# Kernel optimization log

Hardware: AMD Instinct MI355X
Metric: run time of the kernel (lower is better)

## Reference

```python
import jax, jax.numpy as jnp
import numpy as np

OBS, ACT, LAT, H = 64, 32, 25, 5
B = 8192
SUP_H = 64


def setup_inputs() -> dict:
    key = jax.random.key(0)
    ks = jax.random.split(key, 12)
    s = 0.1
    inp = {
        'obs': jax.random.normal(ks[0], (B, OBS), jnp.float32),
        # supervisor FeedForward: OBS -> 64 -> 64 -> LAT, ReLU hidden, Sigmoid output
        'sw1': jax.random.normal(ks[1], (OBS, SUP_H), jnp.float32) * s,
        'sb1': jnp.zeros((SUP_H,), jnp.float32),
        'sw2': jax.random.normal(ks[2], (SUP_H, SUP_H), jnp.float32) * s,
        'sb2': jnp.zeros((SUP_H,), jnp.float32),
        'sw3': jax.random.normal(ks[3], (SUP_H, LAT), jnp.float32) * s,
        'sb3': jnp.zeros((LAT,), jnp.float32),
        # OBS*ACT tiny reflex FeedForwards 1 -> H -> 1, stacked into batched params
        'rw1': jax.random.normal(ks[4], (OBS, ACT, H), jnp.float32) * s,
        'rb1': jnp.zeros((OBS, ACT, H), jnp.float32),
        'rw2': jax.random.normal(ks[5], (OBS, ACT, H), jnp.float32) * s,
        'rb2': jnp.zeros((OBS, ACT), jnp.float32),
        # activation matrix (LAT, OBS, ACT)
        'act_matrix': jnp.ones((LAT, OBS, ACT), jnp.float32),
    }
    return inp


def reference(obs, sw1, sb1, sw2, sb2, sw3, sb3, rw1, rb1, rw2, rb2, act_matrix):
    # supervisor: (B, LAT) sigmoid latent activations
    h = jax.nn.relu(obs @ sw1 + sb1)
    h = jax.nn.relu(h @ sw2 + sb2)
    latent = jax.nn.sigmoid(h @ sw3 + sb3)

    # reflex gating: (B, LAT) x (LAT, OBS, ACT) -> (B, OBS, ACT), softmax over ACT
    logits = jnp.einsum('bl,loa->boa', latent, act_matrix)
    reflex_acts = jax.nn.softmax(logits, axis=-1)

    # all OBS*ACT tiny 1->H->1 MLPs, batched: input is obs[:, o] (scalar per net)
    # hidden: (B, OBS, ACT, H)
    rh = jax.nn.relu(obs[:, :, None, None] * rw1[None] + rb1[None])
    reflex_out = jnp.einsum('boah,oah->boa', rh, rw2) + rb2[None]  # (B, OBS, ACT)

    # weighted sum over obs dim -> (B, ACT)
    return jnp.sum(reflex_out * reflex_acts, axis=1)
```

## Files before the change

kernel.cpp:

```cpp
#include <hip/hip_runtime.h>


#define TOBS 64
#define TACT 32
#define TLAT 25
#define TH   5
#define TB   8192
#define BT   16
#define NCH  16
#define ATS  28
#define WTS  20
#define HSTR 68

#define DPP_ADD(x, ctrl) \
  ((x) + __builtin_bit_cast(float, __builtin_amdgcn_update_dpp( \
      0, __builtin_bit_cast(int, (x)), (ctrl), 0xF, 0xF, true)))

__device__ __forceinline__ float halfwave_sum(float x) {
    x = DPP_ADD(x, 0xB1);
    x = DPP_ADD(x, 0x4E);
    x = DPP_ADD(x, 0x141);
    x = DPP_ADD(x, 0x140);
    int y = __builtin_amdgcn_ds_swizzle(__builtin_bit_cast(int, x), 0x401F);
    return x + __builtin_bit_cast(float, y);
}

__device__ __forceinline__ float sigmoidf_(float x) {
    return 1.0f / (1.0f + __expf(-x));
}

__global__ __launch_bounds__(256, 2)
void reflex_fused(const float* __restrict__ obs,
                  const float* __restrict__ sw1, const float* __restrict__ sb1,
                  const float* __restrict__ sw2, const float* __restrict__ sb2,
                  const float* __restrict__ sw3, const float* __restrict__ sb3,
                  const float* __restrict__ rw1, const float* __restrict__ rb1,
                  const float* __restrict__ rw2, const float* __restrict__ rb2,
                  const float* __restrict__ am,  float* __restrict__ out)
{
    __shared__ __align__(16) float obs_s[BT * HSTR];
    __shared__ __align__(16) float lat_s[BT * 26];
    __shared__ __align__(16) union {
        struct { float h1[BT * HSTR]; float h2[BT * HSTR]; } p1;
        struct { float At[2][128 * ATS]; float W[2][128 * WTS]; } p2;
    } U;

    const int tid  = threadIdx.x;
    const int row0 = blockIdx.x * BT;

    {
        const int r = tid >> 4, f = tid & 15;
        *(float4*)&obs_s[r * HSTR + f * 4] =
            *(const float4*)&obs[(row0 + r) * TOBS + f * 4];
    }
    __syncthreads();

    {
        const int r = tid >> 4, j0 = (tid & 15) * 4;
        float4 acc = *(const float4*)&sb1[j0];
        #pragma unroll 8
        for (int k = 0; k < 64; ++k) {
            float x = obs_s[r * HSTR + k];
            const float4 w = *(const float4*)&sw1[k * 64 + j0];
            acc.x = fmaf(x, w.x, acc.x); acc.y = fmaf(x, w.y, acc.y);
            acc.z = fmaf(x, w.z, acc.z); acc.w = fmaf(x, w.w, acc.w);
        }
        *(float4*)&U.p1.h1[r * HSTR + j0] =
            make_float4(fmaxf(acc.x, 0.f), fmaxf(acc.y, 0.f),
                        fmaxf(acc.z, 0.f), fmaxf(acc.w, 0.f));
    }
    __syncthreads();

    {
        const int r = tid >> 4, j0 = (tid & 15) * 4;
        float4 acc = *(const float4*)&sb2[j0];
        #pragma unroll 8
        for (int k = 0; k < 64; ++k) {
            float x = U.p1.h1[r * HSTR + k];
            const float4 w = *(const float4*)&sw2[k * 64 + j0];
            acc.x = fmaf(x, w.x, acc.x); acc.y = fmaf(x, w.y, acc.y);
            acc.z = fmaf(x, w.z, acc.z); acc.w = fmaf(x, w.w, acc.w);
        }
        *(float4*)&U.p1.h2[r * HSTR + j0] =
            make_float4(fmaxf(acc.x, 0.f), fmaxf(acc.y, 0.f),
                        fmaxf(acc.z, 0.f), fmaxf(acc.w, 0.f));
    }
    __syncthreads();

    {
        const int r = tid >> 4, q = tid & 15;
        if (q < 13) {
            const int j = q * 2;
            float a0 = sb3[j];
            float a1 = (j + 1 < TLAT) ? sb3[j + 1] : 0.f;
            #pragma unroll 8
            for (int k = 0; k < 64; ++k) {
                float x = U.p1.h2[r * HSTR + k];
                a0 = fmaf(x, sw3[k * TLAT + j], a0);
                if (j + 1 < TLAT) a1 = fmaf(x, sw3[k * TLAT + j + 1], a1);
            }
            lat_s[r * 26 + j] = sigmoidf_(a0);
            if (j + 1 < TLAT) lat_s[r * 26 + j + 1] = sigmoidf_(a1);
        }
    }
    __syncthreads();

    const int a  = tid & 31;
    const int hw = tid >> 5;
    const int r0 = hw * 2, r1 = r0 + 1;

    float latA[TLAT], latB[TLAT];
    #pragma unroll
    for (int l = 0; l < TLAT; ++l) {
        latA[l] = lat_s[r0 * 26 + l];
        latB[l] = lat_s[r1 * 26 + l];
    }

    auto stage = [&](int c, int b) {
        if (tid < 128) {
            const int slot = tid >> 5, a_ = tid & 31;
            const int o = c * 4 + slot;
            const float* g = am + o * TACT + a_;
            float v0  = g[0*2048],  v1  = g[1*2048],  v2  = g[2*2048],  v3  = g[3*2048];
            float v4  = g[4*2048],  v5  = g[5*2048],  v6  = g[6*2048],  v7  = g[7*2048];
            float v8  = g[8*2048],  v9  = g[9*2048],  v10 = g[10*2048], v11 = g[11*2048];
            float v12 = g[12*2048], v13 = g[13*2048], v14 = g[14*2048], v15 = g[15*2048];
            float v16 = g[16*2048], v17 = g[17*2048], v18 = g[18*2048], v19 = g[19*2048];
            float v20 = g[20*2048], v21 = g[21*2048], v22 = g[22*2048], v23 = g[23*2048];
            float v24 = g[24*2048];
            float* d = &U.p2.At[b][tid * ATS];
            ((float4*)d)[0] = make_float4(v0,  v1,  v2,  v3);
            ((float4*)d)[1] = make_float4(v4,  v5,  v6,  v7);
            ((float4*)d)[2] = make_float4(v8,  v9,  v10, v11);
            ((float4*)d)[3] = make_float4(v12, v13, v14, v15);
            ((float4*)d)[4] = make_float4(v16, v17, v18, v19);
            ((float4*)d)[5] = make_float4(v20, v21, v22, v23);
            d[24] = v24;
        } else {
            const int t = tid - 128;
            const int slot = t >> 5, a_ = t & 31;
            const int o = c * 4 + slot;
            const int gb = (o * TACT + a_) * TH;
            float w10 = rw1[gb], w11 = rw1[gb+1], w12 = rw1[gb+2], w13 = rw1[gb+3], w14 = rw1[gb+4];
            float b10 = rb1[gb], b11 = rb1[gb+1], b12 = rb1[gb+2], b13 = rb1[gb+3], b14 = rb1[gb+4];
            float w20 = rw2[gb], w21 = rw2[gb+1], w22 = rw2[gb+2], w23 = rw2[gb+3], w24 = rw2[gb+4];
            float b2v = rb2[o * TACT + a_];
            float* d = &U.p2.W[b][t * WTS];
            ((float4*)d)[0] = make_float4(w10, w11, w12, w13);
            ((float4*)d)[1] = make_float4(w14, b10, b11, b12);
            ((float4*)d)[2] = make_float4(b13, b14, w20, w21);
            ((float4*)d)[3] = make_float4(w22, w23, w24, b2v);
        }
    };

    float acc0 = 0.f, acc1 = 0.f;

    stage(0, 0);
    __syncthreads();

    for (int c = 0; c < NCH; ++c) {
        const float* Atb = U.p2.At[c & 1];
        const float* Wb  = U.p2.W[c & 1];
        #pragma unroll
        for (int i = 0; i < 4; ++i) {
            const int o  = c * 4 + i;
            const float* Ap = &Atb[(i * 32 + a) * ATS];
            const float4 A0 = ((const float4*)Ap)[0];
            const float4 A1 = ((const float4*)Ap)[1];
            const float4 A2 = ((const float4*)Ap)[2];
            const float4 A3 = ((const float4*)Ap)[3];
            const float4 A4 = ((const float4*)Ap)[4];
            const float4 A5 = ((const float4*)Ap)[5];
            const float  a24 = Ap[24];

            float l0 = 0.f, l1 = 0.f;
            #define DOT_(comp, idx) \
                l0 = fmaf((comp), latA[idx], l0); l1 = fmaf((comp), latB[idx], l1);
            DOT_(A0.x, 0)  DOT_(A0.y, 1)  DOT_(A0.z, 2)  DOT_(A0.w, 3)
            DOT_(A1.x, 4)  DOT_(A1.y, 5)  DOT_(A1.z, 6)  DOT_(A1.w, 7)
            DOT_(A2.x, 8)  DOT_(A2.y, 9)  DOT_(A2.z, 10) DOT_(A2.w, 11)
            DOT_(A3.x, 12) DOT_(A3.y, 13) DOT_(A3.z, 14) DOT_(A3.w, 15)
            DOT_(A4.x, 16) DOT_(A4.y, 17) DOT_(A4.z, 18) DOT_(A4.w, 19)
            DOT_(A5.x, 20) DOT_(A5.y, 21) DOT_(A5.z, 22) DOT_(A5.w, 23)
            DOT_(a24, 24)
            #undef DOT_

            float e0 = __expf(l0), e1 = __expf(l1);
            float p0 = e0 * __builtin_amdgcn_rcpf(halfwave_sum(e0));
            float p1 = e1 * __builtin_amdgcn_rcpf(halfwave_sum(e1));

            const float* Wp = &Wb[(i * 32 + a) * WTS];
            const float4 W0 = ((const float4*)Wp)[0];
            const float4 W1 = ((const float4*)Wp)[1];
            const float4 W2 = ((const float4*)Wp)[2];
            const float4 W3 = ((const float4*)Wp)[3];

            float x0 = obs_s[r0 * HSTR + o], x1 = obs_s[r1 * HSTR + o];
            float ro0 = W3.w, ro1 = W3.w;
            ro0 = fmaf(fmaxf(fmaf(x0, W0.x, W1.y), 0.f), W2.z, ro0);
            ro1 = fmaf(fmaxf(fmaf(x1, W0.x, W1.y), 0.f), W2.z, ro1);
            ro0 = fmaf(fmaxf(fmaf(x0, W0.y, W1.z), 0.f), W2.w, ro0);
            ro1 = fmaf(fmaxf(fmaf(x1, W0.y, W1.z), 0.f), W2.w, ro1);
            ro0 = fmaf(fmaxf(fmaf(x0, W0.z, W1.w), 0.f), W3.x, ro0);
            ro1 = fmaf(fmaxf(fmaf(x1, W0.z, W1.w), 0.f), W3.x, ro1);
            ro0 = fmaf(fmaxf(fmaf(x0, W0.w, W2.x), 0.f), W3.y, ro0);
            ro1 = fmaf(fmaxf(fmaf(x1, W0.w, W2.x), 0.f), W3.y, ro1);
            ro0 = fmaf(fmaxf(fmaf(x0, W1.x, W2.y), 0.f), W3.z, ro0);
            ro1 = fmaf(fmaxf(fmaf(x1, W1.x, W2.y), 0.f), W3.z, ro1);

            acc0 = fmaf(ro0, p0, acc0);
            acc1 = fmaf(ro1, p1, acc1);
        }
        if (c + 1 < NCH) stage(c + 1, (c + 1) & 1);
        __syncthreads();
    }

    out[(row0 + r0) * TACT + a] = acc0;
    out[(row0 + r1) * TACT + a] = acc1;
}

extern "C" void kernel_launch(void* const* d_in, const int* in_sizes, int n_in,
                              void* d_out, int out_size, void* d_ws, size_t ws_size,
                              hipStream_t stream) {
    const float* obs = (const float*)d_in[0];
    const float* sw1 = (const float*)d_in[1];
    const float* sb1 = (const float*)d_in[2];
    const float* sw2 = (const float*)d_in[3];
    const float* sb2 = (const float*)d_in[4];
    const float* sw3 = (const float*)d_in[5];
    const float* sb3 = (const float*)d_in[6];
    const float* rw1 = (const float*)d_in[7];
    const float* rb1 = (const float*)d_in[8];
    const float* rw2 = (const float*)d_in[9];
    const float* rb2 = (const float*)d_in[10];
    const float* am  = (const float*)d_in[11];
    float* out = (float*)d_out;

    reflex_fused<<<TB / BT, 256, 0, stream>>>(obs, sw1, sb1, sw2, sb2, sw3, sb3,
                                              rw1, rb1, rw2, rb2, am, out);
}
```

Baseline: 53.58 us.

## Split obs dimension across two blocks with atomic reduction and register-prefetched staging

Each batch tile is now handled by two blocks, each covering half of the obs dimension, which doubles the grid. Partial results are combined with atomic adds into an output that is zeroed first with a memset. Staging is spread across all four 64-thread groups and split into a global load issued before compute and a shared-memory write issued after it, so the loads overlap with compute. In exchange, both blocks of a pair recompute the supervisor MLP, and the change adds a memset, atomics, and a non-deterministic summation order.

```diff
diff --git a/kernel.cpp b/kernel.cpp
--- a/kernel.cpp
+++ b/kernel.cpp
@@ -4,7 +4,6 @@
 #define TOBS 64
 #define TACT 32
 #define TLAT 25
-#define TH   5
 #define TB   8192
 #define BT   16
 #define NCH  16
@@ -42,11 +41,13 @@
     __shared__ __align__(16) float lat_s[BT * 26];
     __shared__ __align__(16) union {
         struct { float h1[BT * HSTR]; float h2[BT * HSTR]; } p1;
-        struct { float At[2][128 * ATS]; float W[2][128 * WTS]; } p2;
+        struct { float At[2][64 * ATS]; float W[2][64 * WTS]; } p2;
     } U;
 
-    const int tid  = threadIdx.x;
-    const int row0 = blockIdx.x * BT;
+    const int tid   = threadIdx.x;
+    const int bid   = blockIdx.x;
+    const int row0  = (bid >> 1) * BT;
+    const int obase = (bid & 1) * 32;
 
     {
         const int r = tid >> 4, f = tid & 15;
@@ -116,54 +117,72 @@
         latB[l] = lat_s[r1 * 26 + l];
     }
 
-    auto stage = [&](int c, int b) {
-        if (tid < 128) {
-            const int slot = tid >> 5, a_ = tid & 31;
-            const int o = c * 4 + slot;
-            const float* g = am + o * TACT + a_;
-            float v0  = g[0*2048],  v1  = g[1*2048],  v2  = g[2*2048],  v3  = g[3*2048];
-            float v4  = g[4*2048],  v5  = g[5*2048],  v6  = g[6*2048],  v7  = g[7*2048];
-            float v8  = g[8*2048],  v9  = g[9*2048],  v10 = g[10*2048], v11 = g[11*2048];
-            float v12 = g[12*2048], v13 = g[13*2048], v14 = g[14*2048], v15 = g[15*2048];
-            float v16 = g[16*2048], v17 = g[17*2048], v18 = g[18*2048], v19 = g[19*2048];
-            float v20 = g[20*2048], v21 = g[21*2048], v22 = g[22*2048], v23 = g[23*2048];
-            float v24 = g[24*2048];
-            float* d = &U.p2.At[b][tid * ATS];
-            ((float4*)d)[0] = make_float4(v0,  v1,  v2,  v3);
-            ((float4*)d)[1] = make_float4(v4,  v5,  v6,  v7);
-            ((float4*)d)[2] = make_float4(v8,  v9,  v10, v11);
-            ((float4*)d)[3] = make_float4(v12, v13, v14, v15);
-            ((float4*)d)[4] = make_float4(v16, v17, v18, v19);
-            ((float4*)d)[5] = make_float4(v20, v21, v22, v23);
-            d[24] = v24;
+    const int role = tid >> 6;
+    const int rt   = tid & 63;
+    const int rslot = rt >> 5, ra = rt & 31;
+    float s0, s1, s2, s3, s4, s5, s6, s7, s8, s9, s10, s11, s12;
+
+    auto stage_load = [&](int c) {
+        const int o = obase + c * 2 + rslot;
+        if (role == 0) {
+            const float* g = am + o * TACT + ra;
+            s0 = g[0*2048];  s1 = g[1*2048];  s2  = g[2*2048];  s3  = g[3*2048];
+            s4 = g[4*2048];  s5 = g[5*2048];  s6  = g[6*2048];  s7  = g[7*2048];
+            s8 = g[8*2048];  s9 = g[9*2048];  s10 = g[10*2048]; s11 = g[11*2048];
+        } else if (role == 1) {
+            const float* g = am + o * TACT + ra;
+            s0 = g[12*2048]; s1 = g[13*2048]; s2  = g[14*2048]; s3  = g[15*2048];
+            s4 = g[16*2048]; s5 = g[17*2048]; s6  = g[18*2048]; s7  = g[19*2048];
+            s8 = g[20*2048]; s9 = g[21*2048]; s10 = g[22*2048]; s11 = g[23*2048];
+            s12 = g[24*2048];
+        } else if (role == 2) {
+            const int gb = (o * TACT + ra) * 5;
+            s0 = rw1[gb]; s1 = rw1[gb+1]; s2 = rw1[gb+2]; s3 = rw1[gb+3];
+            s4 = rw1[gb+4]; s5 = rb1[gb]; s6 = rb1[gb+1]; s7 = rb1[gb+2];
         } else {
-            const int t = tid - 128;
-            const int slot = t >> 5, a_ = t & 31;
-            const int o = c * 4 + slot;
-            const int gb = (o * TACT + a_) * TH;
-            float w10 = rw1[gb], w11 = rw1[gb+1], w12 = rw1[gb+2], w13 = rw1[gb+3], w14 = rw1[gb+4];
-            float b10 = rb1[gb], b11 = rb1[gb+1], b12 = rb1[gb+2], b13 = rb1[gb+3], b14 = rb1[gb+4];
-            float w20 = rw2[gb], w21 = rw2[gb+1], w22 = rw2[gb+2], w23 = rw2[gb+3], w24 = rw2[gb+4];
-            float b2v = rb2[o * TACT + a_];
-            float* d = &U.p2.W[b][t * WTS];
-            ((float4*)d)[0] = make_float4(w10, w11, w12, w13);
-            ((float4*)d)[1] = make_float4(w14, b10, b11, b12);
-            ((float4*)d)[2] = make_float4(b13, b14, w20, w21);
-            ((float4*)d)[3] = make_float4(w22, w23, w24, b2v);
+            const int gb = (o * TACT + ra) * 5;
+            s0 = rb1[gb+3]; s1 = rb1[gb+4]; s2 = rw2[gb]; s3 = rw2[gb+1];
+            s4 = rw2[gb+2]; s5 = rw2[gb+3]; s6 = rw2[gb+4]; s7 = rb2[o * TACT + ra];
         }
     };
 
+    auto stage_write = [&](int b) {
+        if (role == 0) {
+            float* d = &U.p2.At[b][rt * ATS];
+            ((float4*)d)[0] = make_float4(s0, s1, s2,  s3);
+            ((float4*)d)[1] = make_float4(s4, s5, s6,  s7);
+            ((float4*)d)[2] = make_float4(s8, s9, s10, s11);
+        } else if (role == 1) {
+            float* d = &U.p2.At[b][rt * ATS];
+            ((float4*)d)[3] = make_float4(s0, s1, s2,  s3);
+            ((float4*)d)[4] = make_float4(s4, s5, s6,  s7);
+            ((float4*)d)[5] = make_float4(s8, s9, s10, s11);
+            d[24] = s12;
+        } else if (role == 2) {
+            float* d = &U.p2.W[b][rt * WTS];
+            ((float4*)d)[0] = make_float4(s0, s1, s2, s3);
+            ((float4*)d)[1] = make_float4(s4, s5, s6, s7);
+        } else {
+            float* d = &U.p2.W[b][rt * WTS];
+            ((float4*)d)[2] = make_float4(s0, s1, s2, s3);
+            ((float4*)d)[3] = make_float4(s4, s5, s6, s7);
+        }
+    };
+
     float acc0 = 0.f, acc1 = 0.f;
 
-    stage(0, 0);
+    stage_load(0);
+    stage_write(0);
     __syncthreads();
 
     for (int c = 0; c < NCH; ++c) {
+        if (c + 1 < NCH) stage_load(c + 1);
+
         const float* Atb = U.p2.At[c & 1];
         const float* Wb  = U.p2.W[c & 1];
         #pragma unroll
-        for (int i = 0; i < 4; ++i) {
-            const int o  = c * 4 + i;
+        for (int i = 0; i < 2; ++i) {
+            const int o  = obase + c * 2 + i;
             const float* Ap = &Atb[(i * 32 + a) * ATS];
             const float4 A0 = ((const float4*)Ap)[0];
             const float4 A1 = ((const float4*)Ap)[1];
@@ -211,12 +230,13 @@
             acc0 = fmaf(ro0, p0, acc0);
             acc1 = fmaf(ro1, p1, acc1);
         }
-        if (c + 1 < NCH) stage(c + 1, (c + 1) & 1);
+
+        if (c + 1 < NCH) stage_write((c + 1) & 1);
         __syncthreads();
     }
 
-    out[(row0 + r0) * TACT + a] = acc0;
-    out[(row0 + r1) * TACT + a] = acc1;
+    unsafeAtomicAdd(&out[(row0 + r0) * TACT + a], acc0);
+    unsafeAtomicAdd(&out[(row0 + r1) * TACT + a], acc1);
 }
 
 extern "C" void kernel_launch(void* const* d_in, const int* in_sizes, int n_in,
@@ -236,6 +256,7 @@
     const float* am  = (const float*)d_in[11];
     float* out = (float*)d_out;
 
-    reflex_fused<<<TB / BT, 256, 0, stream>>>(obs, sw1, sb1, sw2, sb2, sw3, sb3,
-                                              rw1, rb1, rw2, rb2, am, out);
-}
+    hipMemsetAsync(out, 0, (size_t)out_size * sizeof(float), stream);
+    reflex_fused<<<(TB / BT) * 2, 256, 0, stream>>>(obs, sw1, sb1, sw2, sb2, sw3, sb3,
+                                                    rw1, rb1, rw2, rb2, am, out);
+}
```

Result: slower. 76.53 us (+42.8%).

## Stage activation-matrix chunks via async global_load_lds DMA issued before compute

Applied to the files above, without the earlier changes.

Replaces the register-staged gather of act_matrix chunks with per-lane global_load_lds transfers that write directly into the padded LDS layout. Precomputed offsets are kept in registers and advanced each chunk. The next chunk's DMA is issued at the top of the loop so it overlaps the current chunk's compute, with an explicit vmcnt wait before the barrier. The aim is to remove VGPR pressure and the serial load-then-store latency on 128 threads, at the cost of 14 extra offset registers and duplicate loads for the padding slots.

```diff
diff --git a/kernel.cpp b/kernel.cpp
--- a/kernel.cpp
+++ b/kernel.cpp
@@ -4,13 +4,13 @@
 #define TOBS 64
 #define TACT 32
 #define TLAT 25
-#define TH   5
 #define TB   8192
 #define BT   16
 #define NCH  16
 #define ATS  28
 #define WTS  20
 #define HSTR 68
+#define NDMA 14
 
 #define DPP_ADD(x, ctrl) \
   ((x) + __builtin_bit_cast(float, __builtin_amdgcn_update_dpp( \
@@ -28,6 +28,9 @@
 __device__ __forceinline__ float sigmoidf_(float x) {
     return 1.0f / (1.0f + __expf(-x));
 }
+
+typedef __attribute__((address_space(1))) const void* gptr_t;
+typedef __attribute__((address_space(3))) void*       lptr_t;
 
 __global__ __launch_bounds__(256, 2)
 void reflex_fused(const float* __restrict__ obs,
@@ -105,9 +108,11 @@
     }
     __syncthreads();
 
-    const int a  = tid & 31;
-    const int hw = tid >> 5;
-    const int r0 = hw * 2, r1 = r0 + 1;
+    const int a    = tid & 31;
+    const int hw   = tid >> 5;
+    const int r0   = hw * 2, r1 = r0 + 1;
+    const int wid  = tid >> 6;
+    const int lane = tid & 63;
 
     float latA[TLAT], latB[TLAT];
     #pragma unroll
@@ -116,31 +121,34 @@
         latB[l] = lat_s[r1 * 26 + l];
     }
 
-    auto stage = [&](int c, int b) {
-        if (tid < 128) {
-            const int slot = tid >> 5, a_ = tid & 31;
-            const int o = c * 4 + slot;
-            const float* g = am + o * TACT + a_;
-            float v0  = g[0*2048],  v1  = g[1*2048],  v2  = g[2*2048],  v3  = g[3*2048];
-            float v4  = g[4*2048],  v5  = g[5*2048],  v6  = g[6*2048],  v7  = g[7*2048];
-            float v8  = g[8*2048],  v9  = g[9*2048],  v10 = g[10*2048], v11 = g[11*2048];
-            float v12 = g[12*2048], v13 = g[13*2048], v14 = g[14*2048], v15 = g[15*2048];
-            float v16 = g[16*2048], v17 = g[17*2048], v18 = g[18*2048], v19 = g[19*2048];
-            float v20 = g[20*2048], v21 = g[21*2048], v22 = g[22*2048], v23 = g[23*2048];
-            float v24 = g[24*2048];
-            float* d = &U.p2.At[b][tid * ATS];
-            ((float4*)d)[0] = make_float4(v0,  v1,  v2,  v3);
-            ((float4*)d)[1] = make_float4(v4,  v5,  v6,  v7);
-            ((float4*)d)[2] = make_float4(v8,  v9,  v10, v11);
-            ((float4*)d)[3] = make_float4(v12, v13, v14, v15);
-            ((float4*)d)[4] = make_float4(v16, v17, v18, v19);
-            ((float4*)d)[5] = make_float4(v20, v21, v22, v23);
-            d[24] = v24;
-        } else {
+    int atoff[NDMA];
+    #pragma unroll
+    for (int k = 0; k < NDMA; ++k) {
+        int p   = (wid * NDMA + k) * 64 + lane;
+        int row = p / ATS;
+        int l   = p - row * ATS;
+        if (l > 24) l = 24;
+        atoff[k] = l * 2048 + (row >> 5) * 32 + (row & 31);
+    }
+
+    auto stage_dma = [&](int b) {
+        float* lbase = U.p2.At[b];
+        #pragma unroll
+        for (int k = 0; k < NDMA; ++k) {
+            __builtin_amdgcn_global_load_lds(
+                (gptr_t)(am + atoff[k]),
+                (lptr_t)(lbase + (wid * NDMA + k) * 64),
+                4, 0, 0);
+            atoff[k] += 128;
+        }
+    };
+
+    auto stage_w = [&](int c, int b) {
+        if (tid >= 128) {
             const int t = tid - 128;
             const int slot = t >> 5, a_ = t & 31;
             const int o = c * 4 + slot;
-            const int gb = (o * TACT + a_) * TH;
+            const int gb = (o * TACT + a_) * 5;
             float w10 = rw1[gb], w11 = rw1[gb+1], w12 = rw1[gb+2], w13 = rw1[gb+3], w14 = rw1[gb+4];
             float b10 = rb1[gb], b11 = rb1[gb+1], b12 = rb1[gb+2], b13 = rb1[gb+3], b14 = rb1[gb+4];
             float w20 = rw2[gb], w21 = rw2[gb+1], w22 = rw2[gb+2], w23 = rw2[gb+3], w24 = rw2[gb+4];
@@ -155,10 +163,14 @@
 
     float acc0 = 0.f, acc1 = 0.f;
 
-    stage(0, 0);
+    stage_dma(0);
+    stage_w(0, 0);
+    asm volatile("s_waitcnt vmcnt(0)" ::: "memory");
     __syncthreads();
 
     for (int c = 0; c < NCH; ++c) {
+        if (c + 1 < NCH) stage_dma((c + 1) & 1);
+
         const float* Atb = U.p2.At[c & 1];
         const float* Wb  = U.p2.W[c & 1];
         #pragma unroll
@@ -211,7 +223,9 @@
             acc0 = fmaf(ro0, p0, acc0);
             acc1 = fmaf(ro1, p1, acc1);
         }
-        if (c + 1 < NCH) stage(c + 1, (c + 1) & 1);
+
+        if (c + 1 < NCH) stage_w(c + 1, (c + 1) & 1);
+        asm volatile("s_waitcnt vmcnt(0)" ::: "memory");
         __syncthreads();
     }
 
```

Measured after the change: 83.30 us. 1.55x slower.
